# Kernel tuning notes

Measured on AMD Instinct MI355X. Metric: run time of the kernel, lower is better.

## Reference

```python
import jax, jax.numpy as jnp
import numpy as np

T, B, N, N2 = 2048, 32, 1024, 512

def setup_inputs() -> dict:
    key = jax.random.key(0)
    ks = jax.random.split(key, 7)
    s_n = 1.0 / np.sqrt(N)
    s_n2 = 1.0 / np.sqrt(N2)
    return {
        "hyp": jax.random.normal(ks[0], (T, B, N), dtype=jnp.float32),
        "W_w": jax.random.uniform(ks[1], (N2, N), jnp.float32, -s_n, s_n),
        "W_b": jax.random.uniform(ks[2], (N2,), jnp.float32, -s_n, s_n),
        "Wm_w": jax.random.uniform(ks[3], (N2, N), jnp.float32, -s_n, s_n),
        "Wm_b": jax.random.uniform(ks[4], (N2,), jnp.float32, -s_n, s_n),
        "Wh_w": jax.random.uniform(ks[5], (1, N2), jnp.float32, -s_n2, s_n2),
        "Wh_b": jax.random.uniform(ks[6], (1,), jnp.float32, -s_n2, s_n2),
        "dan_hidden_size": N,
        "attention_hidden_size": N2,
    }

def reference(hyp, W_w, W_b, Wm_w, Wm_b, Wh_w, Wh_b, dan_hidden_size, attention_hidden_size):
    # attention_type == 'attention' branch
    m = jnp.mean(hyp, axis=0)                      # [B, N] mean over time
    x = jnp.transpose(hyp, (1, 0, 2))              # [B, T, N]
    hq = jnp.tanh(jnp.einsum('btn,kn->btk', x, W_w) + W_b)        # [B, T, N2]
    hm = jnp.tanh(m @ Wm_w.T + Wm_b)[:, None, :]   # [B, 1, N2]
    h = hq * hm                                    # [B, T, N2]
    score = jnp.einsum('btk,ok->bto', h, Wh_w) + Wh_b  # [B, T, 1]
    a = jax.nn.softmax(score, axis=1)              # softmax over T
    c = jnp.sum(a * x, axis=1)                     # [B, N]
    return c
```

## Files before the change

### kernel.cpp

```cpp
#include <hip/hip_runtime.h>
#include <hip/hip_bf16.h>

#define TDIM 2048
#define BDIM 32
#define NDIM 1024
#define N2DIM 512
#define BN (BDIM * NDIM)
#define LDSP 72
#define NPART 64

typedef float f32x4 __attribute__((ext_vector_type(4)));
typedef __bf16 bf16x8 __attribute__((ext_vector_type(8)));

__device__ __forceinline__ float bf2f(unsigned int u) {
    union { unsigned int i; float f; } c;
    c.i = (u & 0xffffu) << 16;
    return c.f;
}

__device__ __forceinline__ unsigned short f2bf(float f) {
    union { float f; unsigned int i; } c;
    c.f = f;
    unsigned int i = c.i;
    unsigned int r = (i >> 16) & 1u;
    i += 0x7fffu + r;
    return (unsigned short)(i >> 16);
}

__device__ __forceinline__ int detect_f32(const void* wb) {
    const unsigned short* p = (const unsigned short*)wb;
    int cnt = 0;
    #pragma unroll
    for (int i = 0; i < 64; ++i) cnt += ((p[i] & 0x7fffu) <= 0x3D00u) ? 1 : 0;
    return cnt != 64;
}

__device__ __forceinline__ float ldf(const void* p, size_t i, int isf32) {
    if (isf32) return ((const float*)p)[i];
    return bf2f(((const unsigned short*)p)[i]);
}

__device__ __forceinline__ float tanh_fast(float x) {
    float e = __expf(2.0f * x);
    return 1.0f - 2.0f / (e + 1.0f);
}

__device__ __forceinline__ void unpack8(uint4 u, float* f) {
    f[0] = bf2f(u.x); f[1] = bf2f(u.x >> 16);
    f[2] = bf2f(u.y); f[3] = bf2f(u.y >> 16);
    f[4] = bf2f(u.z); f[5] = bf2f(u.z >> 16);
    f[6] = bf2f(u.w); f[7] = bf2f(u.w >> 16);
}

__device__ __forceinline__ void async16(const void* g, void* l) {
    __builtin_amdgcn_global_load_lds(
        (const __attribute__((address_space(1))) void*)g,
        (__attribute__((address_space(3))) void*)l, 16, 0, 0);
}


__global__ __launch_bounds__(256) void k_mean_cvt(const void* __restrict__ hyp,
                                                  const void* __restrict__ W_w,
                                                  const void* __restrict__ wb,
                                                  unsigned short* __restrict__ hyp16,
                                                  unsigned short* __restrict__ W16,
                                                  float* __restrict__ part) {
    const int isf32 = detect_f32(wb);
    const int tc = blockIdx.y;
    if (tc == NPART) {
        int t = blockIdx.x * 256 + threadIdx.x;
        #pragma unroll
        for (int j = 0; j < 16; ++j) {
            int i4 = (j * 8192 + t) * 4;
            if (isf32) {
                float4 v = *(const float4*)((const float*)W_w + i4);
                ushort4 u = { f2bf(v.x), f2bf(v.y), f2bf(v.z), f2bf(v.w) };
                *(ushort4*)(W16 + i4) = u;
            } else {
                *(ushort4*)(W16 + i4) =
                    *(const ushort4*)((const unsigned short*)W_w + i4);
            }
        }
        return;
    }
    const int col4 = (blockIdx.x * 256 + threadIdx.x) * 4;
    float a0 = 0.f, a1 = 0.f, a2 = 0.f, a3 = 0.f;
    if (isf32) {
        const float* h = (const float*)hyp + (size_t)(tc * 32) * BN + col4;
        unsigned short* o = hyp16 + (size_t)(tc * 32) * BN + col4;
        #pragma unroll 8
        for (int tt = 0; tt < 32; ++tt) {
            float4 v = *(const float4*)(h + (size_t)tt * BN);
            a0 += v.x; a1 += v.y; a2 += v.z; a3 += v.w;
            ushort4 u = { f2bf(v.x), f2bf(v.y), f2bf(v.z), f2bf(v.w) };
            *(ushort4*)(o + (size_t)tt * BN) = u;
        }
    } else {
        const unsigned short* h = (const unsigned short*)hyp + (size_t)(tc * 32) * BN + col4;
        unsigned short* o = hyp16 + (size_t)(tc * 32) * BN + col4;
        #pragma unroll 8
        for (int tt = 0; tt < 32; ++tt) {
            ushort4 u = *(const ushort4*)(h + (size_t)tt * BN);
            *(ushort4*)(o + (size_t)tt * BN) = u;
            a0 += bf2f(u.x); a1 += bf2f(u.y); a2 += bf2f(u.z); a3 += bf2f(u.w);
        }
    }
    float4 r = { a0, a1, a2, a3 };
    *(float4*)(part + (size_t)tc * BN + col4) = r;
}

__global__ __launch_bounds__(256) void k_reduce_mean(const float* __restrict__ part,
                                                     float* __restrict__ m) {
    int i4 = (blockIdx.x * 256 + threadIdx.x) * 4;
    float4 s = { 0.f, 0.f, 0.f, 0.f };
    #pragma unroll
    for (int c = 0; c < NPART; ++c) {
        float4 v = *(const float4*)(part + (size_t)c * BN + i4);
        s.x += v.x; s.y += v.y; s.z += v.z; s.w += v.w;
    }
    float k = 1.0f / (float)TDIM;
    float4 r = { s.x * k, s.y * k, s.z * k, s.w * k };
    *(float4*)(m + i4) = r;
}

__global__ __launch_bounds__(256) void k_g(const float* __restrict__ m,
                                           const void* __restrict__ Wm_w,
                                           const void* __restrict__ Wm_b,
                                           const void* __restrict__ Wh_w,
                                           const void* __restrict__ wb,
                                           float* __restrict__ g) {
    const int isf32 = detect_f32(wb);
    int wid  = (blockIdx.x * 256 + threadIdx.x) >> 6;
    int lane = threadIdx.x & 63;
    int b = wid >> 9;
    int k = wid & 511;
    const float* mr = m + (size_t)b * NDIM;
    float s = 0.f;
    if (isf32) {
        const float* wr = (const float*)Wm_w + (size_t)k * NDIM;
        #pragma unroll
        for (int i = 0; i < 4; ++i) {
            int idx = (lane + i * 64) * 4;
            float4 mv = *(const float4*)(mr + idx);
            float4 wv = *(const float4*)(wr + idx);
            s += mv.x * wv.x + mv.y * wv.y + mv.z * wv.z + mv.w * wv.w;
        }
    } else {
        const unsigned short* wr = (const unsigned short*)Wm_w + (size_t)k * NDIM;
        #pragma unroll
        for (int i = 0; i < 4; ++i) {
            int idx = (lane + i * 64) * 4;
            float4 mv = *(const float4*)(mr + idx);
            ushort4 wv = *(const ushort4*)(wr + idx);
            s += mv.x * bf2f(wv.x) + mv.y * bf2f(wv.y)
               + mv.z * bf2f(wv.z) + mv.w * bf2f(wv.w);
        }
    }
    #pragma unroll
    for (int off = 32; off > 0; off >>= 1) s += __shfl_down(s, off, 64);
    if (lane == 0) {
        float v = tanh_fast(s + ldf(Wm_b, k, isf32));
        g[(size_t)b * N2DIM + k] = v * ldf(Wh_w, k, isf32);
    }
}

__global__ __launch_bounds__(256) void k_score(const unsigned short* __restrict__ hyp16,
                                               const unsigned short* __restrict__ W16,
                                               const void* __restrict__ W_b,
                                               const float* __restrict__ g,
                                               float* __restrict__ sp) {
    __shared__ __align__(16) unsigned short sA[2][128 * 64];
    __shared__ __align__(16) unsigned short sW[2][128 * 64];
    float* sRed = (float*)&sA[0][0];

    const int isf32 = detect_f32(W_b);
    const int tid = threadIdx.x;
    const int l   = tid & 63;
    const int w   = tid >> 6;
    const int wt  = w & 1;
    const int wkk = w >> 1;
    const int lm  = l & 15;
    const int lq  = l >> 4;
    const int b   = blockIdx.y;
    const int t0  = blockIdx.x * 128;
    const int kblk = blockIdx.z;

    const int grow = l >> 3;
    const int gkq  = (l & 7) ^ grow;
    const int swz0 = ((lq)     ^ (lm & 7)) * 8;
    const int swz1 = ((4 + lq) ^ (lm & 7)) * 8;

    const unsigned short* Abase = hyp16 + (size_t)t0 * BN + b * NDIM + gkq * 8;
    const unsigned short* Wbase = W16 + (size_t)(kblk * 128) * NDIM + gkq * 8;

    f32x4 acc[4][4];
    #pragma unroll
    for (int mi = 0; mi < 4; ++mi)
        #pragma unroll
        for (int ni = 0; ni < 4; ++ni) {
            f32x4 z = {0.f, 0.f, 0.f, 0.f};
            acc[mi][ni] = z;
        }

    {
        #pragma unroll
        for (int p = 0; p < 4; ++p) {
            const int row = (w * 4 + p) * 8 + grow;
            async16(Abase + (size_t)row * BN, &sA[0][(w * 4 + p) * 512]);
            async16(Wbase + (size_t)row * NDIM, &sW[0][(w * 4 + p) * 512]);
        }
    }

    for (int it = 0; it < 16; ++it) {
        const int cur = it & 1;
        __syncthreads();
        if (it + 1 < 16) {
            const int nxt = cur ^ 1;
            const int n1 = (it + 1) * 64;
            #pragma unroll
            for (int p = 0; p < 4; ++p) {
                const int row = (w * 4 + p) * 8 + grow;
                async16(Abase + (size_t)row * BN + n1, &sA[nxt][(w * 4 + p) * 512]);
                async16(Wbase + (size_t)row * NDIM + n1, &sW[nxt][(w * 4 + p) * 512]);
            }
        }
        #pragma unroll
        for (int kk = 0; kk < 2; ++kk) {
            const int swz = kk ? swz1 : swz0;
            bf16x8 af[4];
            #pragma unroll
            for (int mi = 0; mi < 4; ++mi) {
                int mrow = wt * 64 + mi * 16 + lm;
                af[mi] = *(const bf16x8*)&sA[cur][mrow * 64 + swz];
            }
            #pragma unroll
            for (int ni = 0; ni < 4; ++ni) {
                int nrow = wkk * 64 + ni * 16 + lm;
                bf16x8 bfr = *(const bf16x8*)&sW[cur][nrow * 64 + swz];
                #pragma unroll
                for (int mi = 0; mi < 4; ++mi)
                    acc[mi][ni] = __builtin_amdgcn_mfma_f32_16x16x32_bf16(
                        af[mi], bfr, acc[mi][ni], 0, 0, 0);
            }
        }
    }

    float scoreAcc[4][4];
    #pragma unroll
    for (int mi = 0; mi < 4; ++mi)
        #pragma unroll
        for (int r = 0; r < 4; ++r) scoreAcc[mi][r] = 0.f;
    #pragma unroll
    for (int ni = 0; ni < 4; ++ni) {
        int kc = kblk * 128 + wkk * 64 + ni * 16 + lm;
        float wbv = ldf(W_b, kc, isf32);
        float gg  = g[(size_t)b * N2DIM + kc];
        #pragma unroll
        for (int mi = 0; mi < 4; ++mi)
            #pragma unroll
            for (int r = 0; r < 4; ++r) {
                float v = tanh_fast(acc[mi][ni][r] + wbv);
                scoreAcc[mi][r] += v * gg;
            }
    }

    #pragma unroll
    for (int mi = 0; mi < 4; ++mi)
        #pragma unroll
        for (int r = 0; r < 4; ++r) {
            float s = scoreAcc[mi][r];
            s += __shfl_xor(s, 1, 64);
            s += __shfl_xor(s, 2, 64);
            s += __shfl_xor(s, 4, 64);
            s += __shfl_xor(s, 8, 64);
            if (lm == 0) sRed[wkk * 128 + wt * 64 + mi * 16 + lq * 4 + r] = s;
        }
    __syncthreads();
    if (tid < 128) {
        sp[(size_t)(kblk * BDIM + b) * TDIM + t0 + tid] = sRed[tid] + sRed[128 + tid];
    }
}

__global__ __launch_bounds__(256) void k_softmax(const float* __restrict__ sp,
                                                 float* __restrict__ a) {
    __shared__ float red[8];
    int b = blockIdx.x;
    int tid = threadIdx.x;
    int w = tid >> 6, l = tid & 63;
    float v[8];
    float mx = -1e30f;
    #pragma unroll
    for (int i = 0; i < 8; ++i) {
        int t = tid + i * 256;
        float s = sp[(size_t)(0 * BDIM + b) * TDIM + t]
                + sp[(size_t)(1 * BDIM + b) * TDIM + t]
                + sp[(size_t)(2 * BDIM + b) * TDIM + t]
                + sp[(size_t)(3 * BDIM + b) * TDIM + t];
        v[i] = s; mx = fmaxf(mx, s);
    }
    #pragma unroll
    for (int off = 32; off > 0; off >>= 1) mx = fmaxf(mx, __shfl_xor(mx, off, 64));
    if (l == 0) red[w] = mx;
    __syncthreads();
    mx = fmaxf(fmaxf(red[0], red[1]), fmaxf(red[2], red[3]));
    float sum = 0.f;
    #pragma unroll
    for (int i = 0; i < 8; ++i) { v[i] = __expf(v[i] - mx); sum += v[i]; }
    #pragma unroll
    for (int off = 32; off > 0; off >>= 1) sum += __shfl_xor(sum, off, 64);
    if (l == 0) red[4 + w] = sum;
    __syncthreads();
    sum = red[4] + red[5] + red[6] + red[7];
    float inv = 1.0f / sum;
    float* ap = a + (size_t)b * TDIM;
    #pragma unroll
    for (int i = 0; i < 8; ++i) ap[tid + i * 256] = v[i] * inv;
}

__global__ __launch_bounds__(256) void k_wsum_part(const unsigned short* __restrict__ hyp16,
                                                   const float* __restrict__ a,
                                                   float* __restrict__ part) {
    const int col8 = (blockIdx.x * 256 + threadIdx.x) * 8;
    const int tc   = blockIdx.y;
    const int b    = col8 >> 10;
    const float* av = a + (size_t)b * TDIM + tc * 32;
    const uint4* src = (const uint4*)(hyp16 + (size_t)(tc * 32) * BN + col8);
    float acc[8] = {0.f,0.f,0.f,0.f,0.f,0.f,0.f,0.f};
    #pragma unroll 8
    for (int tt = 0; tt < 32; ++tt) {
        float wgt = av[tt];
        uint4 u = src[(size_t)tt * (BN / 8)];
        float f[8]; unpack8(u, f);
        #pragma unroll
        for (int j = 0; j < 8; ++j) acc[j] += wgt * f[j];
    }
    float* dst = part + (size_t)tc * BN + col8;
    #pragma unroll
    for (int j = 0; j < 8; ++j) dst[j] = acc[j];
}

__global__ __launch_bounds__(256) void k_reduce_out(const float* __restrict__ part,
                                                    const void* __restrict__ wb,
                                                    void* __restrict__ out) {
    const int isf32 = detect_f32(wb);
    int i4 = (blockIdx.x * 256 + threadIdx.x) * 4;
    float4 s = { 0.f, 0.f, 0.f, 0.f };
    #pragma unroll
    for (int c = 0; c < NPART; ++c) {
        float4 v = *(const float4*)(part + (size_t)c * BN + i4);
        s.x += v.x; s.y += v.y; s.z += v.z; s.w += v.w;
    }
    if (isf32) {
        *(float4*)((float*)out + i4) = s;
    } else {
        ushort4 u = { f2bf(s.x), f2bf(s.y), f2bf(s.z), f2bf(s.w) };
        *(ushort4*)((unsigned short*)out + i4) = u;
    }
}

__global__ __launch_bounds__(256) void k_mean_fb(const void* __restrict__ hyp,
                                                 const void* __restrict__ wb,
                                                 float* __restrict__ m) {
    const int isf32 = detect_f32(wb);
    int i = blockIdx.x * 256 + threadIdx.x;
    float s = 0.f;
    if (isf32) {
        const float* h = (const float*)hyp;
        #pragma unroll 8
        for (int t = 0; t < TDIM; ++t) s += h[(size_t)t * BN + i];
    } else {
        const unsigned short* h = (const unsigned short*)hyp;
        #pragma unroll 8
        for (int t = 0; t < TDIM; ++t) s += bf2f(h[(size_t)t * BN + i]);
    }
    m[i] = s * (1.0f / (float)TDIM);
}

__global__ __launch_bounds__(256) void k_score_fb(const void* __restrict__ hyp,
                                                  const void* __restrict__ W_w,
                                                  const void* __restrict__ W_b,
                                                  const float* __restrict__ g,
                                                  float* __restrict__ score) {
    __shared__ __align__(16) unsigned short sA[128 * LDSP];
    __shared__ __align__(16) unsigned short sW[128 * LDSP];
    __shared__ float sRed[2][128];

    const int isf32 = detect_f32(W_b);
    const int tid = threadIdx.x;
    const int l   = tid & 63;
    const int w   = tid >> 6;
    const int wt  = w & 1;
    const int wkk = w >> 1;
    const int lm  = l & 15;
    const int lq  = l >> 4;
    const int b   = blockIdx.y;
    const int t0  = blockIdx.x * 128;

    float scoreAcc[4][4];
    #pragma unroll
    for (int mi = 0; mi < 4; ++mi)
        #pragma unroll
        for (int r = 0; r < 4; ++r) scoreAcc[mi][r] = 0.f;

    for (int kblk = 0; kblk < 4; ++kblk) {
        f32x4 acc[4][4];
        #pragma unroll
        for (int mi = 0; mi < 4; ++mi)
            #pragma unroll
            for (int ni = 0; ni < 4; ++ni) {
                f32x4 z = {0.f, 0.f, 0.f, 0.f};
                acc[mi][ni] = z;
            }
        for (int it = 0; it < 16; ++it) {
            const int n0 = it * 64;
            #pragma unroll
            for (int p = 0; p < 4; ++p) {
                int ch  = p * 256 + tid;
                int row = ch >> 3;
                int pos = ch & 7;
                size_t offA = (size_t)(t0 + row) * BN + b * NDIM + n0 + pos * 8;
                size_t offW = (size_t)(kblk * 128 + row) * NDIM + n0 + pos * 8;
                uint4 va, vw;
                if (isf32) {
                    const float4* fa = (const float4*)((const float*)hyp + offA);
                    float4 a0 = fa[0], a1 = fa[1];
                    va.x = f2bf(a0.x) | ((unsigned)f2bf(a0.y) << 16);
                    va.y = f2bf(a0.z) | ((unsigned)f2bf(a0.w) << 16);
                    va.z = f2bf(a1.x) | ((unsigned)f2bf(a1.y) << 16);
                    va.w = f2bf(a1.z) | ((unsigned)f2bf(a1.w) << 16);
                    const float4* fw = (const float4*)((const float*)W_w + offW);
                    float4 w0 = fw[0], w1 = fw[1];
                    vw.x = f2bf(w0.x) | ((unsigned)f2bf(w0.y) << 16);
                    vw.y = f2bf(w0.z) | ((unsigned)f2bf(w0.w) << 16);
                    vw.z = f2bf(w1.x) | ((unsigned)f2bf(w1.y) << 16);
                    vw.w = f2bf(w1.z) | ((unsigned)f2bf(w1.w) << 16);
                } else {
                    va = *(const uint4*)((const unsigned short*)hyp + offA);
                    vw = *(const uint4*)((const unsigned short*)W_w + offW);
                }
                *(uint4*)&sA[row * LDSP + pos * 8] = va;
                *(uint4*)&sW[row * LDSP + pos * 8] = vw;
            }
            __syncthreads();
            #pragma unroll
            for (int kk = 0; kk < 2; ++kk) {
                const int koff = kk * 32 + lq * 8;
                bf16x8 af[4];
                #pragma unroll
                for (int mi = 0; mi < 4; ++mi) {
                    int mrow = wt * 64 + mi * 16 + lm;
                    af[mi] = *(const bf16x8*)&sA[mrow * LDSP + koff];
                }
                #pragma unroll
                for (int ni = 0; ni < 4; ++ni) {
                    int nrow = wkk * 64 + ni * 16 + lm;
                    bf16x8 bfr = *(const bf16x8*)&sW[nrow * LDSP + koff];
                    #pragma unroll
                    for (int mi = 0; mi < 4; ++mi)
                        acc[mi][ni] = __builtin_amdgcn_mfma_f32_16x16x32_bf16(
                            af[mi], bfr, acc[mi][ni], 0, 0, 0);
                }
            }
            __syncthreads();
        }
        #pragma unroll
        for (int ni = 0; ni < 4; ++ni) {
            int kc = kblk * 128 + wkk * 64 + ni * 16 + lm;
            float wbv = ldf(W_b, kc, isf32);
            float gg  = g[(size_t)b * N2DIM + kc];
            #pragma unroll
            for (int mi = 0; mi < 4; ++mi)
                #pragma unroll
                for (int r = 0; r < 4; ++r) {
                    float v = tanh_fast(acc[mi][ni][r] + wbv);
                    scoreAcc[mi][r] += v * gg;
                }
        }
    }
    #pragma unroll
    for (int mi = 0; mi < 4; ++mi)
        #pragma unroll
        for (int r = 0; r < 4; ++r) {
            float s = scoreAcc[mi][r];
            s += __shfl_xor(s, 1, 64);
            s += __shfl_xor(s, 2, 64);
            s += __shfl_xor(s, 4, 64);
            s += __shfl_xor(s, 8, 64);
            if (lm == 0) sRed[wkk][wt * 64 + mi * 16 + lq * 4 + r] = s;
        }
    __syncthreads();
    if (tid < 128) {
        score[(size_t)b * TDIM + t0 + tid] = sRed[0][tid] + sRed[1][tid];
    }
}

__global__ __launch_bounds__(256) void k_softmax_fb(const float* __restrict__ score,
                                                    float* __restrict__ a) {
    __shared__ float red[8];
    int b = blockIdx.x;
    int tid = threadIdx.x;
    int w = tid >> 6, l = tid & 63;
    const float* s = score + (size_t)b * TDIM;
    float v[8];
    float mx = -1e30f;
    #pragma unroll
    for (int i = 0; i < 8; ++i) { v[i] = s[tid + i * 256]; mx = fmaxf(mx, v[i]); }
    #pragma unroll
    for (int off = 32; off > 0; off >>= 1) mx = fmaxf(mx, __shfl_xor(mx, off, 64));
    if (l == 0) red[w] = mx;
    __syncthreads();
    mx = fmaxf(fmaxf(red[0], red[1]), fmaxf(red[2], red[3]));
    float sum = 0.f;
    #pragma unroll
    for (int i = 0; i < 8; ++i) { v[i] = __expf(v[i] - mx); sum += v[i]; }
    #pragma unroll
    for (int off = 32; off > 0; off >>= 1) sum += __shfl_xor(sum, off, 64);
    if (l == 0) red[4 + w] = sum;
    __syncthreads();
    sum = red[4] + red[5] + red[6] + red[7];
    float inv = 1.0f / sum;
    float* ap = a + (size_t)b * TDIM;
    #pragma unroll
    for (int i = 0; i < 8; ++i) ap[tid + i * 256] = v[i] * inv;
}

__global__ __launch_bounds__(256) void k_wsum_fb(const void* __restrict__ hyp,
                                                 const float* __restrict__ a,
                                                 const void* __restrict__ wb,
                                                 void* __restrict__ out) {
    const int isf32 = detect_f32(wb);
    int i = blockIdx.x * 256 + threadIdx.x;
    int b = i >> 10;
    const float* av = a + (size_t)b * TDIM;
    float s = 0.f;
    if (isf32) {
        const float* h = (const float*)hyp;
        #pragma unroll 8
        for (int t = 0; t < TDIM; ++t) s += av[t] * h[(size_t)t * BN + i];
    } else {
        const unsigned short* h = (const unsigned short*)hyp;
        #pragma unroll 8
        for (int t = 0; t < TDIM; ++t) s += av[t] * bf2f(h[(size_t)t * BN + i]);
    }
    if (isf32) ((float*)out)[i] = s;
    else       ((unsigned short*)out)[i] = f2bf(s);
}

extern "C" void kernel_launch(void* const* d_in, const int* in_sizes, int n_in,
                              void* d_out, int out_size, void* d_ws, size_t ws_size,
                              hipStream_t stream) {
    const void* hyp  = d_in[0];
    const void* W_w  = d_in[1];
    const void* W_b  = d_in[2];
    const void* Wm_w = d_in[3];
    const void* Wm_b = d_in[4];
    const void* Wh_w = d_in[5];

    float* ws    = (float*)d_ws;
    float* m     = ws;
    float* g     = m + BN;
    float* sp    = g + BDIM * N2DIM;
    float* a     = sp + 4 * BDIM * TDIM;
    float* part  = a + BDIM * TDIM;
    unsigned short* W16   = (unsigned short*)(part + NPART * BN);
    unsigned short* hyp16 = W16 + (size_t)N2DIM * NDIM;
    const size_t need = 145162240ull;

    if (ws_size >= need) {
        k_mean_cvt  <<<dim3(32, NPART + 1), 256, 0, stream>>>(hyp, W_w, W_b, hyp16, W16, part);
        k_reduce_mean<<<dim3(32),           256, 0, stream>>>(part, m);
        k_g         <<<dim3(4096),          256, 0, stream>>>(m, Wm_w, Wm_b, Wh_w, W_b, g);
        k_score     <<<dim3(16, 32, 4),     256, 0, stream>>>(hyp16, W16, W_b, g, sp);
        k_softmax   <<<dim3(32),            256, 0, stream>>>(sp, a);
        k_wsum_part <<<dim3(16, NPART),     256, 0, stream>>>(hyp16, a, part);
        k_reduce_out<<<dim3(32),            256, 0, stream>>>(part, W_b, d_out);
    } else {
        float* score = sp;
        k_mean_fb   <<<dim3(128),    256, 0, stream>>>(hyp, W_b, m);
        k_g         <<<dim3(4096),   256, 0, stream>>>(m, Wm_w, Wm_b, Wh_w, W_b, g);
        k_score_fb  <<<dim3(16, 32), 256, 0, stream>>>(hyp, W_w, W_b, g, score);
        k_softmax_fb<<<dim3(32),     256, 0, stream>>>(score, a);
        k_wsum_fb   <<<dim3(128),    256, 0, stream>>>(hyp, a, W_b, d_out);
    }
}
```

Baseline: 563.1 us.

## Load score GEMM operands directly from global into registers, drop LDS staging

```diff
diff --git a/kernel.cpp b/kernel.cpp
--- a/kernel.cpp
+++ b/kernel.cpp
@@ -50,12 +50,6 @@
     f[2] = bf2f(u.y); f[3] = bf2f(u.y >> 16);
     f[4] = bf2f(u.z); f[5] = bf2f(u.z >> 16);
     f[6] = bf2f(u.w); f[7] = bf2f(u.w >> 16);
-}
-
-__device__ __forceinline__ void async16(const void* g, void* l) {
-    __builtin_amdgcn_global_load_lds(
-        (const __attribute__((address_space(1))) void*)g,
-        (__attribute__((address_space(3))) void*)l, 16, 0, 0);
 }
 
 
@@ -169,94 +163,65 @@
                                                const void* __restrict__ W_b,
                                                const float* __restrict__ g,
                                                float* __restrict__ sp) {
-    __shared__ __align__(16) unsigned short sA[2][128 * 64];
-    __shared__ __align__(16) unsigned short sW[2][128 * 64];
-    float* sRed = (float*)&sA[0][0];
+    __shared__ float sRed[2][64];
 
     const int isf32 = detect_f32(W_b);
     const int tid = threadIdx.x;
     const int l   = tid & 63;
     const int w   = tid >> 6;
     const int wt  = w & 1;
-    const int wkk = w >> 1;
+    const int wk  = w >> 1;
     const int lm  = l & 15;
     const int lq  = l >> 4;
     const int b   = blockIdx.y;
-    const int t0  = blockIdx.x * 128;
-    const int kblk = blockIdx.z;
-
-    const int grow = l >> 3;
-    const int gkq  = (l & 7) ^ grow;
-    const int swz0 = ((lq)     ^ (lm & 7)) * 8;
-    const int swz1 = ((4 + lq) ^ (lm & 7)) * 8;
-
-    const unsigned short* Abase = hyp16 + (size_t)t0 * BN + b * NDIM + gkq * 8;
-    const unsigned short* Wbase = W16 + (size_t)(kblk * 128) * NDIM + gkq * 8;
-
-    f32x4 acc[4][4];
-    #pragma unroll
-    for (int mi = 0; mi < 4; ++mi)
-        #pragma unroll
-        for (int ni = 0; ni < 4; ++ni) {
+    const int t0  = blockIdx.x * 64;
+    const int kh  = blockIdx.z;
+
+    const unsigned short* Arow =
+        hyp16 + (size_t)(t0 + wt * 32 + lm) * BN + b * NDIM + lq * 8;
+    const unsigned short* Brow =
+        W16 + (size_t)(kh * 256 + wk * 128 + lm) * NDIM + lq * 8;
+
+    f32x4 acc[2][8];
+    #pragma unroll
+    for (int mi = 0; mi < 2; ++mi)
+        #pragma unroll
+        for (int ni = 0; ni < 8; ++ni) {
             f32x4 z = {0.f, 0.f, 0.f, 0.f};
             acc[mi][ni] = z;
         }
 
-    {
-        #pragma unroll
-        for (int p = 0; p < 4; ++p) {
-            const int row = (w * 4 + p) * 8 + grow;
-            async16(Abase + (size_t)row * BN, &sA[0][(w * 4 + p) * 512]);
-            async16(Wbase + (size_t)row * NDIM, &sW[0][(w * 4 + p) * 512]);
-        }
-    }
-
     for (int it = 0; it < 16; ++it) {
-        const int cur = it & 1;
-        __syncthreads();
-        if (it + 1 < 16) {
-            const int nxt = cur ^ 1;
-            const int n1 = (it + 1) * 64;
-            #pragma unroll
-            for (int p = 0; p < 4; ++p) {
-                const int row = (w * 4 + p) * 8 + grow;
-                async16(Abase + (size_t)row * BN + n1, &sA[nxt][(w * 4 + p) * 512]);
-                async16(Wbase + (size_t)row * NDIM + n1, &sW[nxt][(w * 4 + p) * 512]);
-            }
-        }
         #pragma unroll
         for (int kk = 0; kk < 2; ++kk) {
-            const int swz = kk ? swz1 : swz0;
-            bf16x8 af[4];
-            #pragma unroll
-            for (int mi = 0; mi < 4; ++mi) {
-                int mrow = wt * 64 + mi * 16 + lm;
-                af[mi] = *(const bf16x8*)&sA[cur][mrow * 64 + swz];
-            }
-            #pragma unroll
-            for (int ni = 0; ni < 4; ++ni) {
-                int nrow = wkk * 64 + ni * 16 + lm;
-                bf16x8 bfr = *(const bf16x8*)&sW[cur][nrow * 64 + swz];
+            const int noff = it * 64 + kk * 32;
+            bf16x8 af[2];
+            #pragma unroll
+            for (int mi = 0; mi < 2; ++mi)
+                af[mi] = *(const bf16x8*)(Arow + (size_t)mi * 16 * BN + noff);
+            #pragma unroll
+            for (int ni = 0; ni < 8; ++ni) {
+                bf16x8 bfr = *(const bf16x8*)(Brow + (size_t)ni * 16 * NDIM + noff);
                 #pragma unroll
-                for (int mi = 0; mi < 4; ++mi)
+                for (int mi = 0; mi < 2; ++mi)
                     acc[mi][ni] = __builtin_amdgcn_mfma_f32_16x16x32_bf16(
                         af[mi], bfr, acc[mi][ni], 0, 0, 0);
             }
         }
     }
 
-    float scoreAcc[4][4];
-    #pragma unroll
-    for (int mi = 0; mi < 4; ++mi)
+    float scoreAcc[2][4];
+    #pragma unroll
+    for (int mi = 0; mi < 2; ++mi)
         #pragma unroll
         for (int r = 0; r < 4; ++r) scoreAcc[mi][r] = 0.f;
     #pragma unroll
-    for (int ni = 0; ni < 4; ++ni) {
-        int kc = kblk * 128 + wkk * 64 + ni * 16 + lm;
+    for (int ni = 0; ni < 8; ++ni) {
+        int kc = kh * 256 + wk * 128 + ni * 16 + lm;
         float wbv = ldf(W_b, kc, isf32);
         float gg  = g[(size_t)b * N2DIM + kc];
         #pragma unroll
-        for (int mi = 0; mi < 4; ++mi)
+        for (int mi = 0; mi < 2; ++mi)
             #pragma unroll
             for (int r = 0; r < 4; ++r) {
                 float v = tanh_fast(acc[mi][ni][r] + wbv);
@@ -265,7 +230,7 @@
     }
 
     #pragma unroll
-    for (int mi = 0; mi < 4; ++mi)
+    for (int mi = 0; mi < 2; ++mi)
         #pragma unroll
         for (int r = 0; r < 4; ++r) {
             float s = scoreAcc[mi][r];
@@ -273,11 +238,11 @@
             s += __shfl_xor(s, 2, 64);
             s += __shfl_xor(s, 4, 64);
             s += __shfl_xor(s, 8, 64);
-            if (lm == 0) sRed[wkk * 128 + wt * 64 + mi * 16 + lq * 4 + r] = s;
+            if (lm == 0) sRed[wk][wt * 32 + mi * 16 + lq * 4 + r] = s;
         }
     __syncthreads();
-    if (tid < 128) {
-        sp[(size_t)(kblk * BDIM + b) * TDIM + t0 + tid] = sRed[tid] + sRed[128 + tid];
+    if (tid < 64) {
+        sp[(size_t)(kh * BDIM + b) * TDIM + t0 + tid] = sRed[0][tid] + sRed[1][tid];
     }
 }
 
@@ -293,9 +258,7 @@
     for (int i = 0; i < 8; ++i) {
         int t = tid + i * 256;
         float s = sp[(size_t)(0 * BDIM + b) * TDIM + t]
-                + sp[(size_t)(1 * BDIM + b) * TDIM + t]
-                + sp[(size_t)(2 * BDIM + b) * TDIM + t]
-                + sp[(size_t)(3 * BDIM + b) * TDIM + t];
+                + sp[(size_t)(1 * BDIM + b) * TDIM + t];
         v[i] = s; mx = fmaxf(mx, s);
     }
     #pragma unroll
@@ -570,7 +533,7 @@
         k_mean_cvt  <<<dim3(32, NPART + 1), 256, 0, stream>>>(hyp, W_w, W_b, hyp16, W16, part);
         k_reduce_mean<<<dim3(32),           256, 0, stream>>>(part, m);
         k_g         <<<dim3(4096),          256, 0, stream>>>(m, Wm_w, Wm_b, Wh_w, W_b, g);
-        k_score     <<<dim3(16, 32, 4),     256, 0, stream>>>(hyp16, W16, W_b, g, sp);
+        k_score     <<<dim3(32, 32, 2),     256, 0, stream>>>(hyp16, W16, W_b, g, sp);
         k_softmax   <<<dim3(32),            256, 0, stream>>>(sp, a);
         k_wsum_part <<<dim3(16, NPART),     256, 0, stream>>>(hyp16, a, part);
         k_reduce_out<<<dim3(32),            256, 0, stream>>>(part, W_b, d_out);
```

Measured after the change: 738.6 us. +31.2%, slower.
